# Performance work log

Measured on AMD Instinct MI355X. Metric: run time of the kernel, lower is better.

## Reference

```python
import jax, jax.numpy as jnp
import numpy as np

D_MODEL = 2048
NUM_HEADS = 16
HEAD_DIM = D_MODEL // NUM_HEADS
SCALE = 1.0 / np.sqrt(HEAD_DIM).astype(np.float32)
NEG_INF = -1e9


def setup_inputs() -> dict:
    key = jax.random.key(0)
    ks = jax.random.split(key, 10)
    B, S = 2, 2048
    x = jax.random.normal(ks[0], (B, S, D_MODEL), dtype=jnp.float32)
    # causal lower-triangular mask, broadcastable over (B, H)
    causal_mask = jnp.tril(jnp.ones((S, S), dtype=jnp.int32))[None, None]
    init = 1.0 / np.sqrt(D_MODEL)
    def lin(kw, kb):
        W = jax.random.uniform(kw, (D_MODEL, D_MODEL), jnp.float32, -init, init)
        b = jax.random.uniform(kb, (D_MODEL,), jnp.float32, -init, init)
        return W, b
    Wq, bq = lin(ks[1], ks[2])
    Wk, bk = lin(ks[3], ks[4])
    Wv, bv = lin(ks[5], ks[6])
    Wo, bo = lin(ks[7], ks[8])
    return {"x": x, "causal_mask": causal_mask,
            "Wq": Wq, "bq": bq, "Wk": Wk, "bk": bk,
            "Wv": Wv, "bv": bv, "Wo": Wo, "bo": bo}


def reference(x, causal_mask, Wq, bq, Wk, bk, Wv, bv, Wo, bo):
    B, S, _ = x.shape
    def proj(W, b):
        # torch Linear: x @ W.T + b -> (B, H, S, Dh)
        y = jnp.einsum('bsd,ed->bse', x, W) + b
        return y.reshape(B, S, NUM_HEADS, HEAD_DIM).transpose(0, 2, 1, 3)
    q = proj(Wq, bq)
    k = proj(Wk, bk)
    v = proj(Wv, bv)
    # apply_rope is a no-op stub in the source; q, k unchanged.
    scores = jnp.einsum('bhqd,bhkd->bhqk', q, k) * SCALE
    scores = jnp.where(causal_mask == 0, NEG_INF, scores)
    attn = jax.nn.softmax(scores, axis=-1)
    out = jnp.einsum('bhqk,bhkd->bhqd', attn, v)
    out = out.transpose(0, 2, 1, 3).reshape(B, S, D_MODEL)
    return jnp.einsum('bsd,ed->bse', out, Wo) + bo
```

## Files before the change

### kernel.cpp

```cpp
#include <hip/hip_runtime.h>
#include <hip/hip_bf16.h>
#include <stdint.h>
#include <stddef.h>

typedef __bf16 bf16_t;
typedef __bf16 bf16x4_t __attribute__((ext_vector_type(4)));
typedef __bf16 bf16x8_t __attribute__((ext_vector_type(8)));
typedef float f32x4 __attribute__((ext_vector_type(4)));

#define D_MODEL 2048
#define NHEADS 16
#define HDIM 128
#define SEQ 2048
#define BATCH 2
#define MTOT (BATCH * SEQ)
#define SCALE_F 0.08838834764831845f
#define LOG2E 1.4426950408889634f
#define QSCALE (SCALE_F * LOG2E)
#define KT 32
#define NEGI -3.0e38f
#define MINIT -1.0e30f

#define AS1 __attribute__((address_space(1)))
#define AS3 __attribute__((address_space(3)))

__device__ __forceinline__ void load_lds16(const bf16_t* g, bf16_t* l) {
  __builtin_amdgcn_global_load_lds((AS1 void*)(g), (AS3 void*)(l), 16, 0, 0);
}

__global__ void cast_kernel(const float* __restrict__ src, bf16_t* __restrict__ dst, int n4) {
  int i = blockIdx.x * blockDim.x + threadIdx.x;
  if (i < n4) {
    float4 v = ((const float4*)src)[i];
    bf16x4_t o;
    o.x = (bf16_t)v.x; o.y = (bf16_t)v.y; o.z = (bf16_t)v.z; o.w = (bf16_t)v.w;
    ((bf16x4_t*)dst)[i] = o;
  }
}

__global__ void cast4_kernel(const float* __restrict__ s0, const float* __restrict__ s1,
                             const float* __restrict__ s2, const float* __restrict__ s3,
                             bf16_t* __restrict__ dst, int n4) {
  int i = blockIdx.x * blockDim.x + threadIdx.x;
  int y = blockIdx.y;
  if (i < n4) {
    const float* src = (y == 0) ? s0 : (y == 1) ? s1 : (y == 2) ? s2 : s3;
    float4 v = ((const float4*)src)[i];
    bf16x4_t o;
    o.x = (bf16_t)v.x; o.y = (bf16_t)v.y; o.z = (bf16_t)v.z; o.w = (bf16_t)v.w;
    ((bf16x4_t*)(dst + (size_t)y * D_MODEL * D_MODEL / 4 * 4))[i] = o;
  }
}

__global__ __launch_bounds__(256) void gemm_fused(
    const bf16_t* __restrict__ A, const bf16_t* __restrict__ Bm, int mode,
    const float* __restrict__ bias0, const float* __restrict__ bias1,
    const float* __restrict__ bias2,
    bf16_t* __restrict__ Qo, bf16_t* __restrict__ Ko, bf16_t* __restrict__ Vto,
    float* __restrict__ Out) {
  const int K = 2048;
  __shared__ __align__(16) bf16_t lA[128 * 64];
  __shared__ __align__(16) bf16_t lB[128 * 64];
  const int m0 = blockIdx.x * 128;
  const int n0 = blockIdx.y * 128;
  const int t = threadIdx.x;
  const int w = t >> 6, lane = t & 63;
  const int wm = w & 1, wn = w >> 1;
  const int la = lane & 15, lb = lane >> 4;

  f32x4 acc[4][4];
  f32x4 zero = {0.f, 0.f, 0.f, 0.f};
#pragma unroll
  for (int i = 0; i < 4; i++)
#pragma unroll
    for (int j = 0; j < 4; j++) acc[i][j] = zero;

  const int row0 = t >> 3, cc = t & 7;
  const int ccs = cc ^ (row0 & 7);
  const bf16_t* gA = A + (size_t)(m0 + row0) * K + ccs * 8;
  const bf16_t* gB = Bm + (size_t)(n0 + row0) * K + ccs * 8;
  bf16_t* sA = lA + t * 8;
  bf16_t* sB = lB + t * 8;

  for (int k0 = 0; k0 < K; k0 += 64) {
    __syncthreads();
#pragma unroll
    for (int i = 0; i < 4; i++)
      load_lds16(gA + k0 + (size_t)(32 * i) * K, sA + 2048 * i);
#pragma unroll
    for (int i = 0; i < 4; i++)
      load_lds16(gB + k0 + (size_t)(32 * i) * K, sB + 2048 * i);
    __syncthreads();
#pragma unroll
    for (int ks = 0; ks < 2; ks++) {
      bf16x8_t af[4], bfr[4];
#pragma unroll
      for (int mt = 0; mt < 4; mt++) {
        int row = wm * 64 + mt * 16 + la;
        af[mt] = *(const bf16x8_t*)(lA + row * 64 + (((ks * 4 + lb) ^ (la & 7)) * 8));
      }
#pragma unroll
      for (int nt = 0; nt < 4; nt++) {
        int row = wn * 64 + nt * 16 + la;
        bfr[nt] = *(const bf16x8_t*)(lB + row * 64 + (((ks * 4 + lb) ^ (la & 7)) * 8));
      }
#pragma unroll
      for (int mt = 0; mt < 4; mt++)
#pragma unroll
        for (int nt = 0; nt < 4; nt++)
          acc[mt][nt] = __builtin_amdgcn_mfma_f32_16x16x32_bf16(af[mt], bfr[nt], acc[mt][nt], 0, 0, 0);
    }
  }

  if (mode == 0) {
#pragma unroll
    for (int mt = 0; mt < 4; mt++) {
#pragma unroll
      for (int nt = 0; nt < 4; nt++) {
        int m = m0 + wm * 64 + mt * 16 + lb * 4;
        int n = n0 + wn * 64 + nt * 16 + la;
        int b = m >> 11, s = m & 2047;
        int which = n >> 11, hd = n & 2047;
        int h = hd >> 7, d = hd & 127;
        float bv = (which == 0 ? bias0 : which == 1 ? bias1 : bias2)[hd];
        f32x4 v = acc[mt][nt];
        if (which == 2) {
          bf16_t* dst = Vto + ((size_t)(b * NHEADS + h) * HDIM + d) * SEQ + s;
          bf16x4_t pk;
          pk.x = (bf16_t)(v.x + bv); pk.y = (bf16_t)(v.y + bv);
          pk.z = (bf16_t)(v.z + bv); pk.w = (bf16_t)(v.w + bv);
          *(bf16x4_t*)dst = pk;
        } else {
          float sc = (which == 0) ? QSCALE : 1.0f;
          bf16_t* dst = (which == 0 ? Qo : Ko) + ((size_t)(b * NHEADS + h) * SEQ + s) * HDIM + d;
          dst[0]        = (bf16_t)((v.x + bv) * sc);
          dst[HDIM]     = (bf16_t)((v.y + bv) * sc);
          dst[2 * HDIM] = (bf16_t)((v.z + bv) * sc);
          dst[3 * HDIM] = (bf16_t)((v.w + bv) * sc);
        }
      }
    }
  } else {
#pragma unroll
    for (int mt = 0; mt < 4; mt++) {
#pragma unroll
      for (int nt = 0; nt < 4; nt++) {
        int m = m0 + wm * 64 + mt * 16 + lb * 4;
        int n = n0 + wn * 64 + nt * 16 + la;
        float bv = bias0[n];
        f32x4 v = acc[mt][nt];
        float* dst = Out + (size_t)m * D_MODEL + n;
        dst[0]           = v.x + bv;
        dst[D_MODEL]     = v.y + bv;
        dst[2 * D_MODEL] = v.z + bv;
        dst[3 * D_MODEL] = v.w + bv;
      }
    }
  }
}

__global__ __launch_bounds__(256, 3) void flash_attn(
    const bf16_t* __restrict__ Q, const bf16_t* __restrict__ Kg,
    const bf16_t* __restrict__ Vt, bf16_t* __restrict__ O,
    bf16_t* __restrict__ PO, float* __restrict__ ML) {
  __shared__ __align__(16) bf16_t lK[2][KT * 128];
  __shared__ __align__(16) bf16_t lV[2][128 * KT];
  __shared__ __align__(16) bf16_t lP[128 * 40];
  const int g = blockIdx.x;
  const int bh = g & 31, idx = g >> 5;
  const int t = threadIdx.x;
  const int w = t >> 6, lane = t & 63;
  const int la = lane & 15, lb = lane >> 4;
  const int qloc = w * 32 + la;

  const bf16_t* Qb = Q + (size_t)bh * SEQ * HDIM;
  const bf16_t* Kb = Kg + (size_t)bh * SEQ * HDIM;
  const bf16_t* Vb = Vt + (size_t)bh * HDIM * SEQ;
  const int b = bh >> 4, h = bh & 15;

  int nph, qts[2], k0s[2], k1s[2], slots[2];
  bool parts[2];
  if (idx < 8) {
    nph = 1; qts[0] = 8 + idx; k0s[0] = 0; k1s[0] = 34;
    parts[0] = true; slots[0] = (idx * 32 + bh) * 2;
  } else {
    int qtA = idx - 8;
    nph = 2;
    qts[0] = qtA; k0s[0] = 0; k1s[0] = 4 * qtA + 4; parts[0] = false; slots[0] = 0;
    qts[1] = 15 - qtA; k0s[1] = 34; k1s[1] = 64 - 4 * qtA;
    parts[1] = true; slots[1] = ((7 - qtA) * 32 + bh) * 2 + 1;
  }

  const int kj = t >> 4, kcc = t & 15;
  const int vd = t >> 2, vjc = t & 3;

  for (int ph = 0; ph < nph; ph++) {
    const int qt = qts[ph], kt0 = k0s[ph], kt1 = k1s[ph];
    const int q0 = qt * 128;

    bf16x8_t qf[2][4];
#pragma unroll
    for (int mt = 0; mt < 2; mt++)
#pragma unroll
      for (int ks = 0; ks < 4; ks++)
        qf[mt][ks] = *(const bf16x8_t*)(Qb + (size_t)(q0 + qloc + mt * 16) * HDIM + ks * 32 + lb * 8);

    f32x4 oacc[2][8];
    float mr[2] = {MINIT, MINIT}, lr[2] = {0.f, 0.f};
    f32x4 zero = {0.f, 0.f, 0.f, 0.f};
#pragma unroll
    for (int mt = 0; mt < 2; mt++)
#pragma unroll
      for (int dt = 0; dt < 8; dt++) oacc[mt][dt] = zero;

    __syncthreads();
    {
      const int j0 = kt0 * KT;
      int buf = kt0 & 1;
#pragma unroll
      for (int i = 0; i < 2; i++) {
        int j = kj + 16 * i;
        load_lds16(Kb + (size_t)(j0 + j) * HDIM + (((kcc ^ (j & 15))) * 8),
                   lK[buf] + (t + 256 * i) * 8);
      }
#pragma unroll
      for (int i = 0; i < 2; i++) {
        int d = vd + 64 * i;
        load_lds16(Vb + (size_t)d * SEQ + j0 + (((vjc ^ ((d & 3) ^ ((d >> 2) & 3)))) * 8),
                   lV[buf] + (t + 256 * i) * 8);
      }
    }

    for (int kt = kt0; kt < kt1; kt++) {
      const int j0 = kt * KT;
      const int cur = kt & 1;
      __syncthreads();

      if (kt + 1 < kt1) {
        const int jn = (kt + 1) * KT;
        const int nb = cur ^ 1;
#pragma unroll
        for (int i = 0; i < 2; i++) {
          int j = kj + 16 * i;
          load_lds16(Kb + (size_t)(jn + j) * HDIM + (((kcc ^ (j & 15))) * 8),
                     lK[nb] + (t + 256 * i) * 8);
        }
#pragma unroll
        for (int i = 0; i < 2; i++) {
          int d = vd + 64 * i;
          load_lds16(Vb + (size_t)d * SEQ + jn + (((vjc ^ ((d & 3) ^ ((d >> 2) & 3)))) * 8),
                     lV[nb] + (t + 256 * i) * 8);
        }
      }

      f32x4 st[2][2];
#pragma unroll
      for (int nt = 0; nt < 2; nt++)
#pragma unroll
        for (int mt = 0; mt < 2; mt++) st[nt][mt] = zero;
#pragma unroll
      for (int ks = 0; ks < 4; ks++) {
#pragma unroll
        for (int nt = 0; nt < 2; nt++) {
          int j = nt * 16 + la;
          int ck = (ks * 4 + lb) ^ (j & 15);
          bf16x8_t kf = *(const bf16x8_t*)(lK[cur] + j * 128 + ck * 8);
#pragma unroll
          for (int mt = 0; mt < 2; mt++)
            st[nt][mt] = __builtin_amdgcn_mfma_f32_16x16x32_bf16(kf, qf[mt][ks], st[nt][mt], 0, 0, 0);
        }
      }

      const bool dm = (j0 + KT > q0);
#pragma unroll
      for (int mt = 0; mt < 2; mt++) {
        int qg = q0 + qloc + mt * 16;
        if (dm) {
#pragma unroll
          for (int nt = 0; nt < 2; nt++)
#pragma unroll
            for (int r = 0; r < 4; r++)
              if (j0 + nt * 16 + lb * 4 + r > qg) st[nt][mt][r] = NEGI;
        }
        float tm = NEGI;
#pragma unroll
        for (int nt = 0; nt < 2; nt++)
#pragma unroll
          for (int r = 0; r < 4; r++) tm = fmaxf(tm, st[nt][mt][r]);
        tm = fmaxf(tm, __shfl_xor(tm, 16));
        tm = fmaxf(tm, __shfl_xor(tm, 32));
        float mnew = fmaxf(mr[mt], tm);
        float alpha = exp2f(mr[mt] - mnew);
        mr[mt] = mnew;
        lr[mt] *= alpha;
#pragma unroll
        for (int dt = 0; dt < 8; dt++) oacc[mt][dt] *= alpha;
        float s = 0.f;
#pragma unroll
        for (int nt = 0; nt < 2; nt++) {
          f32x4 p;
#pragma unroll
          for (int r = 0; r < 4; r++) {
            p[r] = exp2f(st[nt][mt][r] - mnew);
            s += p[r];
          }
          bf16x4_t pk;
          pk.x = (bf16_t)p[0]; pk.y = (bf16_t)p[1]; pk.z = (bf16_t)p[2]; pk.w = (bf16_t)p[3];
          *(bf16x4_t*)(lP + (qloc + mt * 16) * 40 + nt * 16 + lb * 4) = pk;
        }
        s += __shfl_xor(s, 16);
        s += __shfl_xor(s, 32);
        lr[mt] += s;
      }

      bf16x8_t pf[2];
#pragma unroll
      for (int mt = 0; mt < 2; mt++)
        pf[mt] = *(const bf16x8_t*)(lP + (w * 32 + mt * 16 + la) * 40 + lb * 8);
#pragma unroll
      for (int dt = 0; dt < 8; dt++) {
        int d = dt * 16 + la;
        int jc = lb ^ ((d & 3) ^ ((d >> 2) & 3));
        bf16x8_t vf = *(const bf16x8_t*)(lV[cur] + d * 32 + jc * 8);
#pragma unroll
        for (int mt = 0; mt < 2; mt++)
          oacc[mt][dt] = __builtin_amdgcn_mfma_f32_16x16x32_bf16(vf, pf[mt], oacc[mt][dt], 0, 0, 0);
      }
    }

    if (!parts[ph]) {
#pragma unroll
      for (int mt = 0; mt < 2; mt++) {
        float inv = 1.0f / lr[mt];
        int q = q0 + qloc + mt * 16;
        bf16_t* dst = O + ((size_t)b * SEQ + q) * D_MODEL + h * HDIM + lb * 4;
#pragma unroll
        for (int dt = 0; dt < 8; dt++) {
          f32x4 v = oacc[mt][dt];
          bf16x4_t pk;
          pk.x = (bf16_t)(v[0] * inv); pk.y = (bf16_t)(v[1] * inv);
          pk.z = (bf16_t)(v[2] * inv); pk.w = (bf16_t)(v[3] * inv);
          *(bf16x4_t*)(dst + dt * 16) = pk;
        }
      }
    } else {
      const int slot = slots[ph];
      bf16_t* pob = PO + (size_t)slot * 128 * 128;
#pragma unroll
      for (int mt = 0; mt < 2; mt++) {
        int q = qloc + mt * 16;
        bf16_t* dst = pob + (size_t)q * 128 + lb * 4;
#pragma unroll
        for (int dt = 0; dt < 8; dt++) {
          f32x4 v = oacc[mt][dt];
          bf16x4_t pk;
          pk.x = (bf16_t)v[0]; pk.y = (bf16_t)v[1];
          pk.z = (bf16_t)v[2]; pk.w = (bf16_t)v[3];
          *(bf16x4_t*)(dst + dt * 16) = pk;
        }
        if (lb == 0) {
          float2 ml = make_float2(mr[mt], lr[mt]);
          *(float2*)(ML + ((size_t)slot * 128 + q) * 2) = ml;
        }
      }
    }
  }
}

__global__ void merge_kernel(const bf16_t* __restrict__ PO, const float* __restrict__ ML,
                             bf16_t* __restrict__ O) {
  const int qti = blockIdx.x >> 5, bh = blockIdx.x & 31;
  const int qt = 8 + qti;
  const int t = threadIdx.x;
  const int q = t >> 1, dh = (t & 1) * 64;
  const size_t s1 = ((size_t)(qti * 32 + bh)) * 2;
  const float* ml1 = ML + (s1 * 128 + q) * 2;
  const float* ml2 = ML + ((s1 + 1) * 128 + q) * 2;
  float m1 = ml1[0], l1 = ml1[1], m2 = ml2[0], l2 = ml2[1];
  float m = fmaxf(m1, m2);
  float w1 = exp2f(m1 - m), w2 = exp2f(m2 - m);
  float inv = 1.0f / (w1 * l1 + w2 * l2);
  w1 *= inv; w2 *= inv;
  const bf16_t* p1 = PO + (s1 * 128 + q) * 128 + dh;
  const bf16_t* p2 = PO + ((s1 + 1) * 128 + q) * 128 + dh;
  const int b = bh >> 4, h = bh & 15;
  bf16_t* dst = O + ((size_t)b * SEQ + qt * 128 + q) * D_MODEL + h * HDIM + dh;
#pragma unroll
  for (int i = 0; i < 8; i++) {
    bf16x8_t a = ((const bf16x8_t*)p1)[i];
    bf16x8_t c = ((const bf16x8_t*)p2)[i];
    bf16x8_t o;
#pragma unroll
    for (int e = 0; e < 8; e++)
      o[e] = (bf16_t)(w1 * (float)a[e] + w2 * (float)c[e]);
    ((bf16x8_t*)dst)[i] = o;
  }
}

extern "C" void kernel_launch(void* const* d_in, const int* in_sizes, int n_in,
                              void* d_out, int out_size, void* d_ws, size_t ws_size,
                              hipStream_t stream) {
  (void)in_sizes; (void)n_in; (void)out_size; (void)ws_size;
  const float* x  = (const float*)d_in[0];
  const float* Wq = (const float*)d_in[2];
  const float* bq = (const float*)d_in[3];
  const float* Wk = (const float*)d_in[4];
  const float* bk = (const float*)d_in[5];
  const float* Wv = (const float*)d_in[6];
  const float* bv = (const float*)d_in[7];
  const float* Wo = (const float*)d_in[8];
  const float* bo = (const float*)d_in[9];
  float* out = (float*)d_out;

  const size_t NBF = (size_t)MTOT * D_MODEL * sizeof(bf16_t);
  const size_t WBF = (size_t)D_MODEL * D_MODEL * sizeof(bf16_t);
  char* p = (char*)d_ws;
  bf16_t* xb   = (bf16_t*)p; p += NBF;
  bf16_t* Wcat = (bf16_t*)p; p += 4 * WBF;
  bf16_t* Qb   = (bf16_t*)p; p += NBF;
  bf16_t* Kb   = (bf16_t*)p; p += NBF;
  bf16_t* Vtb  = (bf16_t*)p; p += NBF;
  bf16_t* Wob  = Wcat + (size_t)3 * D_MODEL * D_MODEL;
  bf16_t* Ob   = xb;
  bf16_t* PO = Wcat;
  float*  ML = (float*)(Wcat + (size_t)512 * 128 * 128);

  const int WN4 = D_MODEL * D_MODEL / 4;
  const int XN4 = MTOT * D_MODEL / 4;
  cast_kernel<<<XN4 / 256, 256, 0, stream>>>(x, xb, XN4);
  cast4_kernel<<<dim3(WN4 / 256, 4), 256, 0, stream>>>(Wq, Wk, Wv, Wo, Wcat, WN4);

  gemm_fused<<<dim3(MTOT / 128, 6144 / 128), 256, 0, stream>>>(
      xb, Wcat, 0, bq, bk, bv, Qb, Kb, Vtb, nullptr);

  flash_attn<<<dim3(512), 256, 0, stream>>>(Qb, Kb, Vtb, Ob, PO, ML);
  merge_kernel<<<dim3(256), 256, 0, stream>>>(PO, ML, Ob);

  gemm_fused<<<dim3(MTOT / 128, D_MODEL / 128), 256, 0, stream>>>(
      Ob, Wob, 1, bo, nullptr, nullptr, nullptr, nullptr, nullptr, out);
}
```

Baseline: 405.9 us.

## Load K/V tiles directly from global into registers, dropping LDS staging

Replaces the LDS double-buffered K/V staging with per-warp direct global loads into registers. K fragments are prefetched two tiles ahead in ping-pong register sets, and V fragments are loaded at the start of each step. This removes the per-tile __syncthreads and the LDS write/read traffic, but each of the four warps now reloads the full K/V tiles from global/L2, a 4x increase in global reads. Register pressure also rises, so launch bounds drop from 3 to 2 blocks per CU.

```diff
diff --git a/kernel.cpp b/kernel.cpp
--- a/kernel.cpp
+++ b/kernel.cpp
@@ -159,12 +159,94 @@
   }
 }
 
-__global__ __launch_bounds__(256, 3) void flash_attn(
+#define FLASH_STEP(KU, ktc)                                                              \
+  {                                                                                      \
+    const int j0s = (ktc) * KT;                                                          \
+                                            \
+    _Pragma("unroll")                                                                    \
+    for (int dt = 0; dt < 8; dt++)                                                       \
+      vf[dt] = *(const bf16x8_t*)(Vb + (size_t)(dt * 16 + la) * SEQ + j0s + lb * 8);     \
+                                                                        \
+    f32x4 st[2][2];                                                                      \
+    _Pragma("unroll")                                                                    \
+    for (int nt = 0; nt < 2; nt++)                                                       \
+      _Pragma("unroll")                                                                  \
+      for (int mt = 0; mt < 2; mt++) st[nt][mt] = zero;                                  \
+    _Pragma("unroll")                                                                    \
+    for (int ks = 0; ks < 4; ks++)                                                       \
+      _Pragma("unroll")                                                                  \
+      for (int nt = 0; nt < 2; nt++)                                                     \
+        _Pragma("unroll")                                                                \
+        for (int mt = 0; mt < 2; mt++)                                                   \
+          st[nt][mt] = __builtin_amdgcn_mfma_f32_16x16x32_bf16(KU[ks * 2 + nt],          \
+                          qf[mt][ks], st[nt][mt], 0, 0, 0);                              \
+              \
+    {                                                                                    \
+      int jp = (ktc + 2) * KT; if (jp > SEQ - KT) jp = SEQ - KT;                         \
+      _Pragma("unroll")                                                                  \
+      for (int ks = 0; ks < 4; ks++)                                                     \
+        _Pragma("unroll")                                                                \
+        for (int nt = 0; nt < 2; nt++)                                                   \
+          KU[ks * 2 + nt] = *(const bf16x8_t*)(Kb + (size_t)(jp + nt * 16 + la) * HDIM   \
+                                               + (ks * 4 + lb) * 8);                     \
+    }                                                                                    \
+                            \
+    const bool dmk = (j0s + KT > q0);                                                    \
+    _Pragma("unroll")                                                                    \
+    for (int mt = 0; mt < 2; mt++) {                                                     \
+      int qg = q0 + qloc + mt * 16;                                                      \
+      if (dmk) {                                                                         \
+        _Pragma("unroll")                                                                \
+        for (int nt = 0; nt < 2; nt++)                                                   \
+          _Pragma("unroll")                                                              \
+          for (int r = 0; r < 4; r++)                                                    \
+            if (j0s + nt * 16 + lb * 4 + r > qg) st[nt][mt][r] = NEGI;                   \
+      }                                                                                  \
+      float tm = NEGI;                                                                   \
+      _Pragma("unroll")                                                                  \
+      for (int nt = 0; nt < 2; nt++)                                                     \
+        _Pragma("unroll")                                                                \
+        for (int r = 0; r < 4; r++) tm = fmaxf(tm, st[nt][mt][r]);                       \
+      tm = fmaxf(tm, __shfl_xor(tm, 16));                                                \
+      tm = fmaxf(tm, __shfl_xor(tm, 32));                                                \
+      float mnew = fmaxf(mr[mt], tm);                                                    \
+      float alpha = exp2f(mr[mt] - mnew);                                                \
+      mr[mt] = mnew;                                                                     \
+      lr[mt] *= alpha;                                                                   \
+      _Pragma("unroll")                                                                  \
+      for (int dt = 0; dt < 8; dt++) oacc[mt][dt] *= alpha;                              \
+      float s = 0.f;                                                                     \
+      _Pragma("unroll")                                                                  \
+      for (int nt = 0; nt < 2; nt++) {                                                   \
+        f32x4 pv;                                                                        \
+        _Pragma("unroll")                                                                \
+        for (int r = 0; r < 4; r++) { pv[r] = exp2f(st[nt][mt][r] - mnew); s += pv[r]; } \
+        bf16x4_t pk;                                                                     \
+        pk.x = (bf16_t)pv[0]; pk.y = (bf16_t)pv[1];                                      \
+        pk.z = (bf16_t)pv[2]; pk.w = (bf16_t)pv[3];                                      \
+        *(bf16x4_t*)(lP + (qloc + mt * 16) * 40 + nt * 16 + lb * 4) = pk;                \
+      }                                                                                  \
+      s += __shfl_xor(s, 16);                                                            \
+      s += __shfl_xor(s, 32);                                                            \
+      lr[mt] += s;                                                                       \
+    }                                                                                    \
+        \
+    bf16x8_t pf[2];                                                                      \
+    _Pragma("unroll")                                                                    \
+    for (int mt = 0; mt < 2; mt++)                                                       \
+      pf[mt] = *(const bf16x8_t*)(lP + (qloc + mt * 16) * 40 + lb * 8);                  \
+    _Pragma("unroll")                                                                    \
+    for (int dt = 0; dt < 8; dt++)                                                       \
+      _Pragma("unroll")                                                                  \
+      for (int mt = 0; mt < 2; mt++)                                                     \
+        oacc[mt][dt] = __builtin_amdgcn_mfma_f32_16x16x32_bf16(vf[dt], pf[mt],           \
+                          oacc[mt][dt], 0, 0, 0);                                        \
+  }
+
+__global__ __launch_bounds__(256, 2) void flash_attn(
     const bf16_t* __restrict__ Q, const bf16_t* __restrict__ Kg,
     const bf16_t* __restrict__ Vt, bf16_t* __restrict__ O,
     bf16_t* __restrict__ PO, float* __restrict__ ML) {
-  __shared__ __align__(16) bf16_t lK[2][KT * 128];
-  __shared__ __align__(16) bf16_t lV[2][128 * KT];
   __shared__ __align__(16) bf16_t lP[128 * 40];
   const int g = blockIdx.x;
   const int bh = g & 31, idx = g >> 5;
@@ -191,9 +273,6 @@
     parts[1] = true; slots[1] = ((7 - qtA) * 32 + bh) * 2 + 1;
   }
 
-  const int kj = t >> 4, kcc = t & 15;
-  const int vd = t >> 2, vjc = t & 3;
-
   for (int ph = 0; ph < nph; ph++) {
     const int qt = qts[ph], kt0 = k0s[ph], kt1 = k1s[ph];
     const int q0 = qt * 128;
@@ -213,119 +292,22 @@
 #pragma unroll
       for (int dt = 0; dt < 8; dt++) oacc[mt][dt] = zero;
 
-    __syncthreads();
+    bf16x8_t kfA[8], kfB[8], vf[8];
     {
-      const int j0 = kt0 * KT;
-      int buf = kt0 & 1;
-#pragma unroll
-      for (int i = 0; i < 2; i++) {
-        int j = kj + 16 * i;
-        load_lds16(Kb + (size_t)(j0 + j) * HDIM + (((kcc ^ (j & 15))) * 8),
-                   lK[buf] + (t + 256 * i) * 8);
-      }
-#pragma unroll
-      for (int i = 0; i < 2; i++) {
-        int d = vd + 64 * i;
-        load_lds16(Vb + (size_t)d * SEQ + j0 + (((vjc ^ ((d & 3) ^ ((d >> 2) & 3)))) * 8),
-                   lV[buf] + (t + 256 * i) * 8);
-      }
-    }
-
-    for (int kt = kt0; kt < kt1; kt++) {
-      const int j0 = kt * KT;
-      const int cur = kt & 1;
-      __syncthreads();
-
-      if (kt + 1 < kt1) {
-        const int jn = (kt + 1) * KT;
-        const int nb = cur ^ 1;
-#pragma unroll
-        for (int i = 0; i < 2; i++) {
-          int j = kj + 16 * i;
-          load_lds16(Kb + (size_t)(jn + j) * HDIM + (((kcc ^ (j & 15))) * 8),
-                     lK[nb] + (t + 256 * i) * 8);
+      const int jA = kt0 * KT;
+      int jB = (kt0 + 1) * KT; if (jB > SEQ - KT) jB = SEQ - KT;
+#pragma unroll
+      for (int ks = 0; ks < 4; ks++)
+#pragma unroll
+        for (int nt = 0; nt < 2; nt++) {
+          kfA[ks * 2 + nt] = *(const bf16x8_t*)(Kb + (size_t)(jA + nt * 16 + la) * HDIM + (ks * 4 + lb) * 8);
+          kfB[ks * 2 + nt] = *(const bf16x8_t*)(Kb + (size_t)(jB + nt * 16 + la) * HDIM + (ks * 4 + lb) * 8);
         }
-#pragma unroll
-        for (int i = 0; i < 2; i++) {
-          int d = vd + 64 * i;
-          load_lds16(Vb + (size_t)d * SEQ + jn + (((vjc ^ ((d & 3) ^ ((d >> 2) & 3)))) * 8),
-                     lV[nb] + (t + 256 * i) * 8);
-        }
-      }
-
-      f32x4 st[2][2];
-#pragma unroll
-      for (int nt = 0; nt < 2; nt++)
-#pragma unroll
-        for (int mt = 0; mt < 2; mt++) st[nt][mt] = zero;
-#pragma unroll
-      for (int ks = 0; ks < 4; ks++) {
-#pragma unroll
-        for (int nt = 0; nt < 2; nt++) {
-          int j = nt * 16 + la;
-          int ck = (ks * 4 + lb) ^ (j & 15);
-          bf16x8_t kf = *(const bf16x8_t*)(lK[cur] + j * 128 + ck * 8);
-#pragma unroll
-          for (int mt = 0; mt < 2; mt++)
-            st[nt][mt] = __builtin_amdgcn_mfma_f32_16x16x32_bf16(kf, qf[mt][ks], st[nt][mt], 0, 0, 0);
-        }
-      }
-
-      const bool dm = (j0 + KT > q0);
-#pragma unroll
-      for (int mt = 0; mt < 2; mt++) {
-        int qg = q0 + qloc + mt * 16;
-        if (dm) {
-#pragma unroll
-          for (int nt = 0; nt < 2; nt++)
-#pragma unroll
-            for (int r = 0; r < 4; r++)
-              if (j0 + nt * 16 + lb * 4 + r > qg) st[nt][mt][r] = NEGI;
-        }
-        float tm = NEGI;
-#pragma unroll
-        for (int nt = 0; nt < 2; nt++)
-#pragma unroll
-          for (int r = 0; r < 4; r++) tm = fmaxf(tm, st[nt][mt][r]);
-        tm = fmaxf(tm, __shfl_xor(tm, 16));
-        tm = fmaxf(tm, __shfl_xor(tm, 32));
-        float mnew = fmaxf(mr[mt], tm);
-        float alpha = exp2f(mr[mt] - mnew);
-        mr[mt] = mnew;
-        lr[mt] *= alpha;
-#pragma unroll
-        for (int dt = 0; dt < 8; dt++) oacc[mt][dt] *= alpha;
-        float s = 0.f;
-#pragma unroll
-        for (int nt = 0; nt < 2; nt++) {
-          f32x4 p;
-#pragma unroll
-          for (int r = 0; r < 4; r++) {
-            p[r] = exp2f(st[nt][mt][r] - mnew);
-            s += p[r];
-          }
-          bf16x4_t pk;
-          pk.x = (bf16_t)p[0]; pk.y = (bf16_t)p[1]; pk.z = (bf16_t)p[2]; pk.w = (bf16_t)p[3];
-          *(bf16x4_t*)(lP + (qloc + mt * 16) * 40 + nt * 16 + lb * 4) = pk;
-        }
-        s += __shfl_xor(s, 16);
-        s += __shfl_xor(s, 32);
-        lr[mt] += s;
-      }
-
-      bf16x8_t pf[2];
-#pragma unroll
-      for (int mt = 0; mt < 2; mt++)
-        pf[mt] = *(const bf16x8_t*)(lP + (w * 32 + mt * 16 + la) * 40 + lb * 8);
-#pragma unroll
-      for (int dt = 0; dt < 8; dt++) {
-        int d = dt * 16 + la;
-        int jc = lb ^ ((d & 3) ^ ((d >> 2) & 3));
-        bf16x8_t vf = *(const bf16x8_t*)(lV[cur] + d * 32 + jc * 8);
-#pragma unroll
-        for (int mt = 0; mt < 2; mt++)
-          oacc[mt][dt] = __builtin_amdgcn_mfma_f32_16x16x32_bf16(vf, pf[mt], oacc[mt][dt], 0, 0, 0);
-      }
+    }
+
+    for (int kt = kt0; kt < kt1; kt += 2) {
+      FLASH_STEP(kfA, kt);
+      if (kt + 1 < kt1) FLASH_STEP(kfB, kt + 1);
     }
 
     if (!parts[ph]) {
```

New measurement: 453.8 us. 1.12x slower.

## Split paired causal attention work into three equal pieces per block

Applied to the files above, without the earlier changes.

Reworks the flash-attention work split. Each pair of complementary query tiles (qt, 15-qt) has 68 key chunks of combined causal work, which is now cut into three roughly equal ranges of 23 chunks, giving 768 blocks instead of 512. This is meant to balance load across CUs and improve occupancy. The merge kernel now combines two or three partial segments per query tile, and the partial outputs are stored in the output buffer while the M/L statistics live in the weight workspace, which adds more partial traffic and merge work.

```diff
diff --git a/kernel.cpp b/kernel.cpp
--- a/kernel.cpp
+++ b/kernel.cpp
@@ -167,7 +167,13 @@
   __shared__ __align__(16) bf16_t lV[2][128 * KT];
   __shared__ __align__(16) bf16_t lP[128 * 40];
   const int g = blockIdx.x;
-  const int bh = g & 31, idx = g >> 5;
+  const int bh = g & 31, pc = g >> 5;
+  const int pair = pc / 3, piece = pc % 3;
+  const int nA = 4 * pair + 4;
+  const int lo = (piece == 0) ? 0 : ((piece == 1) ? 23 : 46);
+  const int hi = (piece == 2) ? 68 : (lo + 23);
+  const int baseP = (pair < 5) ? (3 * pair) : (15 + 4 * (pair - 5));
+
   const int t = threadIdx.x;
   const int w = t >> 6, lane = t & 63;
   const int la = lane & 15, lb = lane >> 4;
@@ -178,17 +184,26 @@
   const bf16_t* Vb = Vt + (size_t)bh * HDIM * SEQ;
   const int b = bh >> 4, h = bh & 15;
 
-  int nph, qts[2], k0s[2], k1s[2], slots[2];
+  int nph = 0, qts[2], k0s[2], k1s[2], slots[2];
   bool parts[2];
-  if (idx < 8) {
-    nph = 1; qts[0] = 8 + idx; k0s[0] = 0; k1s[0] = 34;
-    parts[0] = true; slots[0] = (idx * 32 + bh) * 2;
-  } else {
-    int qtA = idx - 8;
-    nph = 2;
-    qts[0] = qtA; k0s[0] = 0; k1s[0] = 4 * qtA + 4; parts[0] = false; slots[0] = 0;
-    qts[1] = 15 - qtA; k0s[1] = 34; k1s[1] = 64 - 4 * qtA;
-    parts[1] = true; slots[1] = ((7 - qtA) * 32 + bh) * 2 + 1;
+  {
+    int k0 = lo, k1 = (hi < nA) ? hi : nA;
+    if (k1 > k0) {
+      qts[nph] = pair; k0s[nph] = k0; k1s[nph] = k1;
+      parts[nph] = !(k0 == 0 && k1 == nA);
+      slots[nph] = bh * 27 + baseP + piece;
+      nph++;
+    }
+  }
+  {
+    int k0 = ((lo > nA) ? lo : nA) - nA, k1 = hi - nA;
+    if (k1 > k0) {
+      qts[nph] = 15 - pair; k0s[nph] = k0; k1s[nph] = k1;
+      parts[nph] = true;
+      int localB = (pair < 5) ? piece : (piece + 1);
+      slots[nph] = bh * 27 + baseP + localB;
+      nph++;
+    }
   }
 
   const int kj = t >> 4, kcc = t & 15;
@@ -316,7 +331,7 @@
       bf16x8_t pf[2];
 #pragma unroll
       for (int mt = 0; mt < 2; mt++)
-        pf[mt] = *(const bf16x8_t*)(lP + (w * 32 + mt * 16 + la) * 40 + lb * 8);
+        pf[mt] = *(const bf16x8_t*)(lP + (qloc + mt * 16) * 40 + lb * 8);
 #pragma unroll
       for (int dt = 0; dt < 8; dt++) {
         int d = dt * 16 + la;
@@ -369,30 +384,55 @@
 
 __global__ void merge_kernel(const bf16_t* __restrict__ PO, const float* __restrict__ ML,
                              bf16_t* __restrict__ O) {
-  const int qti = blockIdx.x >> 5, bh = blockIdx.x & 31;
-  const int qt = 8 + qti;
+  const int bhi = blockIdx.x;
+  const int bh = bhi / 11, mi = bhi % 11;
+  int qt, nseg, s0;
+  if (mi < 5) {
+    qt = 15 - mi; nseg = 3; s0 = 3 * mi;
+  } else {
+    int j = mi - 5;
+    int pair = 5 + (j >> 1);
+    bool isB = (j & 1) != 0;
+    qt = isB ? (15 - pair) : pair;
+    nseg = 2;
+    s0 = 15 + 4 * (pair - 5) + (isB ? 2 : 0);
+  }
+  s0 += bh * 27;
   const int t = threadIdx.x;
   const int q = t >> 1, dh = (t & 1) * 64;
-  const size_t s1 = ((size_t)(qti * 32 + bh)) * 2;
-  const float* ml1 = ML + (s1 * 128 + q) * 2;
-  const float* ml2 = ML + ((s1 + 1) * 128 + q) * 2;
-  float m1 = ml1[0], l1 = ml1[1], m2 = ml2[0], l2 = ml2[1];
-  float m = fmaxf(m1, m2);
-  float w1 = exp2f(m1 - m), w2 = exp2f(m2 - m);
-  float inv = 1.0f / (w1 * l1 + w2 * l2);
-  w1 *= inv; w2 *= inv;
-  const bf16_t* p1 = PO + (s1 * 128 + q) * 128 + dh;
-  const bf16_t* p2 = PO + ((s1 + 1) * 128 + q) * 128 + dh;
+
+  float m0 = ML[((size_t)s0 * 128 + q) * 2],       l0 = ML[((size_t)s0 * 128 + q) * 2 + 1];
+  float m1 = ML[((size_t)(s0 + 1) * 128 + q) * 2], l1 = ML[((size_t)(s0 + 1) * 128 + q) * 2 + 1];
+  float m2 = MINIT, l2 = 0.f;
+  if (nseg == 3) {
+    m2 = ML[((size_t)(s0 + 2) * 128 + q) * 2];
+    l2 = ML[((size_t)(s0 + 2) * 128 + q) * 2 + 1];
+  }
+  float m = fmaxf(fmaxf(m0, m1), m2);
+  float w0 = exp2f(m0 - m), w1 = exp2f(m1 - m), w2 = (nseg == 3) ? exp2f(m2 - m) : 0.f;
+  float inv = 1.0f / (w0 * l0 + w1 * l1 + w2 * l2);
+  w0 *= inv; w1 *= inv; w2 *= inv;
+
+  const bf16_t* p0 = PO + ((size_t)s0 * 128 + q) * 128 + dh;
+  const bf16_t* p1 = PO + ((size_t)(s0 + 1) * 128 + q) * 128 + dh;
+  const bf16_t* p2 = PO + ((size_t)(s0 + 2) * 128 + q) * 128 + dh;
   const int b = bh >> 4, h = bh & 15;
   bf16_t* dst = O + ((size_t)b * SEQ + qt * 128 + q) * D_MODEL + h * HDIM + dh;
 #pragma unroll
   for (int i = 0; i < 8; i++) {
-    bf16x8_t a = ((const bf16x8_t*)p1)[i];
-    bf16x8_t c = ((const bf16x8_t*)p2)[i];
+    bf16x8_t a = ((const bf16x8_t*)p0)[i];
+    bf16x8_t c = ((const bf16x8_t*)p1)[i];
     bf16x8_t o;
-#pragma unroll
-    for (int e = 0; e < 8; e++)
-      o[e] = (bf16_t)(w1 * (float)a[e] + w2 * (float)c[e]);
+    if (nseg == 3) {
+      bf16x8_t e = ((const bf16x8_t*)p2)[i];
+#pragma unroll
+      for (int k = 0; k < 8; k++)
+        o[k] = (bf16_t)(w0 * (float)a[k] + w1 * (float)c[k] + w2 * (float)e[k]);
+    } else {
+#pragma unroll
+      for (int k = 0; k < 8; k++)
+        o[k] = (bf16_t)(w0 * (float)a[k] + w1 * (float)c[k]);
+    }
     ((bf16x8_t*)dst)[i] = o;
   }
 }
@@ -422,8 +462,8 @@
   bf16_t* Vtb  = (bf16_t*)p; p += NBF;
   bf16_t* Wob  = Wcat + (size_t)3 * D_MODEL * D_MODEL;
   bf16_t* Ob   = xb;
-  bf16_t* PO = Wcat;
-  float*  ML = (float*)(Wcat + (size_t)512 * 128 * 128);
+  bf16_t* PO = (bf16_t*)d_out;
+  float*  ML = (float*)Wcat;
 
   const int WN4 = D_MODEL * D_MODEL / 4;
   const int XN4 = MTOT * D_MODEL / 4;
@@ -433,8 +473,8 @@
   gemm_fused<<<dim3(MTOT / 128, 6144 / 128), 256, 0, stream>>>(
       xb, Wcat, 0, bq, bk, bv, Qb, Kb, Vtb, nullptr);
 
-  flash_attn<<<dim3(512), 256, 0, stream>>>(Qb, Kb, Vtb, Ob, PO, ML);
-  merge_kernel<<<dim3(256), 256, 0, stream>>>(PO, ML, Ob);
+  flash_attn<<<dim3(768), 256, 0, stream>>>(Qb, Kb, Vtb, Ob, PO, ML);
+  merge_kernel<<<dim3(352), 256, 0, stream>>>(PO, ML, Ob);
 
   gemm_fused<<<dim3(MTOT / 128, D_MODEL / 128), 256, 0, stream>>>(
       Ob, Wob, 1, bo, nullptr, nullptr, nullptr, nullptr, nullptr, out);
```

New measurement: 407.8 us. About the same (+0.5%).
